# Kernel optimization log

Hardware: AMD Instinct MI355X
Metric: run time of the kernel (lower is better)

The kernel has to match this reference:

```python
import jax, jax.numpy as jnp
import numpy as np

B, S, D, H = 4, 8192, 1024, 16
HD = D // H  # head_dim = 64

def elu_feature_map(x):
    return jax.nn.elu(x) + 1.0

def setup_inputs() -> dict:
    key = jax.random.key(0)
    k1, k2, k3 = jax.random.split(key, 3)
    x = jax.random.normal(k1, (B, S, D), dtype=jnp.float32)
    w_qkv = jax.random.normal(k2, (3 * D, D), dtype=jnp.float32) * (D ** -0.5)
    w_out = jax.random.normal(k3, (D, D), dtype=jnp.float32) * (D ** -0.5)
    return {"x": x, "w_qkv": w_qkv, "w_out": w_out}

def reference(x, w_qkv, w_out):
    Bv, Sv, Dv = x.shape
    # qkv projection (torch Linear: x @ W.T), reshape to [3,B,H,S,hd]
    qkv = (x @ w_qkv.T).reshape(Bv, Sv, 3, H, HD)
    qkv = jnp.transpose(qkv, (2, 0, 3, 1, 4))
    q, k, v = qkv[0], qkv[1], qkv[2]
    q = elu_feature_map(q)
    k = elu_feature_map(k)
    # kv state: [B,H,hd,hd]
    kv = jnp.einsum('bhsd,bhse->bhde', k, v)
    out = jnp.einsum('bhsd,bhde->bhse', q, kv)
    k_sum = k.sum(axis=2)  # [B,H,hd]
    normalizer = jnp.einsum('bhsd,bhd->bhs', q, k_sum)[..., None]
    normalizer = jnp.maximum(normalizer, 1e-6)
    out = (out / normalizer).transpose(0, 2, 1, 3).reshape(Bv, Sv, Dv)
    return out @ w_out.T
```

## Files before the change

### kernel.cpp

```cpp
#include <hip/hip_runtime.h>
#include <cstdint>
#include <cstddef>


typedef __bf16 bf16;
typedef __bf16 bf16x8 __attribute__((ext_vector_type(8)));
typedef float  f32x4  __attribute__((ext_vector_type(4)));

#define MFMA(a, b, c) __builtin_amdgcn_mfma_f32_16x16x32_bf16((a), (b), (c), 0, 0, 0)

__device__ __forceinline__ void gld_lds16(const bf16* g, bf16* l) {
  __builtin_amdgcn_global_load_lds(
      (const __attribute__((address_space(1))) void*)g,
      (__attribute__((address_space(3))) void*)l, 16, 0, 0);
}

__global__ __launch_bounds__(256) void cvt_bf16(const float* __restrict__ src,
                                                bf16* __restrict__ dst, int n8) {
  const int stride = gridDim.x * 256;
  for (int i = blockIdx.x * 256 + threadIdx.x; i < n8; i += stride) {
    const float* p = src + (size_t)i * 8;
    f32x4 a = *(const f32x4*)p;
    f32x4 b = *(const f32x4*)(p + 4);
    bf16x8 r;
    r[0] = (bf16)a[0]; r[1] = (bf16)a[1]; r[2] = (bf16)a[2]; r[3] = (bf16)a[3];
    r[4] = (bf16)b[0]; r[5] = (bf16)b[1]; r[6] = (bf16)b[2]; r[7] = (bf16)b[3];
    *(bf16x8*)(dst + (size_t)i * 8) = r;
  }
}

template<int SLAB, bool ST, bool LAST>
__device__ __forceinline__ void ktile(
    const bf16* vA, const bf16* vB, bf16* sA, bf16* sB,
    const bf16* gA, const bf16* gB0, const bf16* gB1,
    f32x4 (&acc)[8][4]) {
  constexpr int NS = (SLAB + 2) % 3;
  constexpr int CB = SLAB * 12288;
  if (!LAST) asm volatile("s_waitcnt vmcnt(6)" ::: "memory");
  else       asm volatile("s_waitcnt vmcnt(0)" ::: "memory");
  __builtin_amdgcn_s_barrier();
  __builtin_amdgcn_sched_barrier(0);

  bf16x8 bv[4], af[4];
#pragma unroll
  for (int nf = 0; nf < 4; ++nf)
    bv[nf] = *(const bf16x8*)&vB[CB + nf * 512];
#pragma unroll
  for (int i = 0; i < 4; ++i)
    af[i] = *(const bf16x8*)&vA[CB + i * 512];
  if (ST) {
    gld_lds16(gA,         sA + NS * 12288);
    gld_lds16(gA + 65536, sA + NS * 12288 + 2048);
    gld_lds16(gB0,        sB + NS * 12288);
  }
  __builtin_amdgcn_s_barrier();
  asm volatile("s_waitcnt lgkmcnt(0)" ::: "memory");
  __builtin_amdgcn_sched_barrier(0);
  __builtin_amdgcn_s_setprio(1);
#pragma unroll
  for (int i = 0; i < 4; ++i)
#pragma unroll
    for (int nf = 0; nf < 4; ++nf)
      acc[i][nf] = MFMA(af[i], bv[nf], acc[i][nf]);
  __builtin_amdgcn_s_setprio(0);
  __builtin_amdgcn_s_barrier();

#pragma unroll
  for (int i = 0; i < 4; ++i)
    af[i] = *(const bf16x8*)&vA[CB + 2048 + i * 512];
  if (ST) {
    gld_lds16(gA + 131072, sA + NS * 12288 + 4096);
    gld_lds16(gA + 196608, sA + NS * 12288 + 6144);
    gld_lds16(gB1,         sB + NS * 12288 + 2048);
  }
  __builtin_amdgcn_s_barrier();
  asm volatile("s_waitcnt lgkmcnt(0)" ::: "memory");
  __builtin_amdgcn_sched_barrier(0);
  __builtin_amdgcn_s_setprio(1);
#pragma unroll
  for (int i = 0; i < 4; ++i)
#pragma unroll
    for (int nf = 0; nf < 4; ++nf)
      acc[4 + i][nf] = MFMA(af[i], bv[nf], acc[4 + i][nf]);
  __builtin_amdgcn_s_setprio(0);
  __builtin_amdgcn_s_barrier();
}

__device__ __forceinline__ void kloop(
    bf16* smem, const bf16* pA, const bf16* pB0, const bf16* pB1,
    int tid, int arow, int brow, int cgo, f32x4 (&acc)[8][4]) {
  bf16* sA = smem + tid * 8;
  bf16* sB = smem + 8192 + tid * 8;
#pragma unroll
  for (int t = 0; t < 2; ++t) {
    const int kk = t * 32;
    gld_lds16(pA + kk,          sA + t * 12288);
    gld_lds16(pA + kk + 65536,  sA + t * 12288 + 2048);
    gld_lds16(pA + kk + 131072, sA + t * 12288 + 4096);
    gld_lds16(pA + kk + 196608, sA + t * 12288 + 6144);
    gld_lds16(pB0 + kk,         sB + t * 12288);
    gld_lds16(pB1 + kk,         sB + t * 12288 + 2048);
  }
  const bf16* vA = smem + arow * 32 + cgo;
  const bf16* vB = smem + 8192 + brow * 32 + cgo;
#pragma unroll
  for (int c = 0; c < 10; ++c) {
    const int o = 64 + c * 96;
    ktile<0, true, false>(vA, vB, sA, sB, pA + o,      pB0 + o,      pB1 + o,      acc);
    ktile<1, true, false>(vA, vB, sA, sB, pA + o + 32, pB0 + o + 32, pB1 + o + 32, acc);
    ktile<2, true, false>(vA, vB, sA, sB, pA + o + 64, pB0 + o + 64, pB1 + o + 64, acc);
  }
  ktile<0, false, false>(vA, vB, sA, sB, pA, pB0, pB1, acc);
  ktile<1, false, true >(vA, vB, sA, sB, pA, pB0, pB1, acc);
}

__global__ __launch_bounds__(256, 2) void gemm_kvfold(
    const bf16* __restrict__ xb, const bf16* __restrict__ wbq,
    float* __restrict__ Pp, float* __restrict__ KsP) {
  __shared__ __align__(16) bf16 smem[36864];
  const int tid = threadIdx.x;
  const int w = tid >> 6, lane = tid & 63;
  const int grp = lane >> 4, mlane = lane & 15;
  const int wm = w >> 1, wn = w & 1;

  int bid = (int)blockIdx.x;
  const int cpx = (int)gridDim.x >> 3;
  bid = (bid & 7) * cpx + (bid >> 3);
  const int h = bid & 15, rt = bid >> 4;
  const int rowA0 = rt * 256;

  const int lrr = tid >> 2;
  const int lcs = (tid & 3) ^ ((tid >> 3) & 3);
  const bf16* pA  = xb + (size_t)(rowA0 + lrr) * 1024 + lcs * 8;
  const bf16* pB0 = wbq + (size_t)(1024 + h * 64 + lrr) * 1024 + lcs * 8;
  const bf16* pB1 = wbq + (size_t)(2048 + h * 64 + lrr) * 1024 + lcs * 8;
  const int cgo = (grp ^ ((mlane >> 1) & 3)) * 8;
  const int arow = wm * 128 + mlane;
  const int brow = wn * 64 + mlane;

  const f32x4 zero = {0.f, 0.f, 0.f, 0.f};
  f32x4 acc[8][4];
#pragma unroll
  for (int i = 0; i < 8; ++i)
#pragma unroll
    for (int j = 0; j < 4; ++j) acc[i][j] = zero;

  kloop(smem, pA, pB0, pB1, tid, arow, brow, cgo, acc);

  bf16* Kt = smem;
  bf16* Vt = smem + 17408;
  {
    bf16* T = wn ? Vt : Kt;
#pragma unroll
    for (int mf = 0; mf < 8; ++mf)
#pragma unroll
      for (int nf = 0; nf < 4; ++nf)
#pragma unroll
        for (int r = 0; r < 4; ++r) {
          float v = acc[mf][nf][r];
          if (wn == 0) v = (v > 0.f) ? (v + 1.f) : __expf(v);
          T[(wm * 128 + mf * 16 + grp * 4 + r) * 68 + nf * 16 + mlane] = (bf16)v;
        }
  }
  __syncthreads();

  f32x4 akv[4][4], a5[4];
#pragma unroll
  for (int i = 0; i < 4; ++i) {
    a5[i] = zero;
#pragma unroll
    for (int j = 0; j < 4; ++j) akv[i][j] = zero;
  }
  bf16x8 ones;
#pragma unroll
  for (int jj = 0; jj < 8; ++jj) ones[jj] = (bf16)1.0f;

#pragma unroll
  for (int c = 0; c < 2; ++c) {
    const int sw = w * 64 + c * 32;
    bf16x8 av[4], bk[4];
#pragma unroll
    for (int jj = 0; jj < 8; ++jj) {
      const bf16* vr = &Vt[(sw + grp * 8 + jj) * 68];
      const bf16* kr = &Kt[(sw + grp * 8 + jj) * 68];
#pragma unroll
      for (int i = 0; i < 4; ++i) av[i][jj] = vr[i * 16 + mlane];
#pragma unroll
      for (int j = 0; j < 4; ++j) bk[j][jj] = kr[j * 16 + mlane];
    }
#pragma unroll
    for (int i = 0; i < 4; ++i)
#pragma unroll
      for (int j = 0; j < 4; ++j) akv[i][j] = MFMA(av[i], bk[j], akv[i][j]);
#pragma unroll
    for (int j = 0; j < 4; ++j) a5[j] = MFMA(ones, bk[j], a5[j]);
  }
  __syncthreads();

  float* Pr = (float*)smem;
  float* Kr = Pr + 8192;
  if (w >= 2) {
#pragma unroll
    for (int i = 0; i < 4; ++i)
#pragma unroll
      for (int j = 0; j < 4; ++j)
#pragma unroll
        for (int r = 0; r < 4; ++r)
          Pr[(w - 2) * 4096 + (i * 16 + grp * 4 + r) * 64 + j * 16 + mlane] =
              akv[i][j][r];
    if (grp == 0) {
#pragma unroll
      for (int j = 0; j < 4; ++j) Kr[(w - 2) * 64 + j * 16 + mlane] = a5[j][0];
    }
  }
  __syncthreads();
  if (w < 2) {
#pragma unroll
    for (int i = 0; i < 4; ++i)
#pragma unroll
      for (int j = 0; j < 4; ++j)
#pragma unroll
        for (int r = 0; r < 4; ++r)
          akv[i][j][r] += Pr[w * 4096 + (i * 16 + grp * 4 + r) * 64 + j * 16 + mlane];
    if (grp == 0) {
#pragma unroll
      for (int j = 0; j < 4; ++j) a5[j][0] += Kr[w * 64 + j * 16 + mlane];
    }
  }
  __syncthreads();
  if (w == 1) {
#pragma unroll
    for (int i = 0; i < 4; ++i)
#pragma unroll
      for (int j = 0; j < 4; ++j)
#pragma unroll
        for (int r = 0; r < 4; ++r)
          Pr[(i * 16 + grp * 4 + r) * 64 + j * 16 + mlane] = akv[i][j][r];
    if (grp == 0) {
#pragma unroll
      for (int j = 0; j < 4; ++j) Kr[j * 16 + mlane] = a5[j][0];
    }
  }
  __syncthreads();
  if (w == 0) {
    const int widx = rt * 16 + h;
    float* pw = Pp + (size_t)widx * 4096;
#pragma unroll
    for (int i = 0; i < 4; ++i)
#pragma unroll
      for (int j = 0; j < 4; ++j)
#pragma unroll
        for (int r = 0; r < 4; ++r)
          pw[(i * 16 + grp * 4 + r) * 64 + j * 16 + mlane] =
              akv[i][j][r] + Pr[(i * 16 + grp * 4 + r) * 64 + j * 16 + mlane];
    if (grp == 0) {
#pragma unroll
      for (int j = 0; j < 4; ++j)
        KsP[(size_t)widx * 64 + j * 16 + mlane] =
            a5[j][0] + Kr[j * 16 + mlane];
    }
  }
}

__global__ __launch_bounds__(256) void reduce_kv2(
    const float* __restrict__ Pp, const float* __restrict__ KsP,
    bf16* __restrict__ kvb, bf16* __restrict__ ksb) {
  const int bh = blockIdx.x, y = blockIdx.y, tid = threadIdx.x;
  const int b = bh >> 4, h = bh & 15;
  if (y < 16) {
    const int o = y * 256 + tid;
    float s = 0.f;
#pragma unroll
    for (int i = 0; i < 32; ++i)
      s += Pp[(size_t)((b * 32 + i) * 16 + h) * 4096 + o];
    kvb[(size_t)bh * 4096 + o] = (bf16)s;
  } else if (tid < 64) {
    float s = 0.f;
#pragma unroll
    for (int i = 0; i < 32; ++i)
      s += KsP[(size_t)((b * 32 + i) * 16 + h) * 64 + tid];
    ksb[bh * 64 + tid] = (bf16)s;
  }
}

__global__ __launch_bounds__(256, 2) void gemm_qattn(
    const bf16* __restrict__ xb, const bf16* __restrict__ wbq,
    const bf16* __restrict__ kvb, const bf16* __restrict__ ksb,
    bf16* __restrict__ attn) {
  __shared__ __align__(16) bf16 smem[36864];
  const int tid = threadIdx.x;
  const int w = tid >> 6, lane = tid & 63;
  const int grp = lane >> 4, mlane = lane & 15;
  const int wm = w >> 1, wn = w & 1;

  int bid = (int)blockIdx.x;
  const int cpx = (int)gridDim.x >> 3;
  bid = (bid & 7) * cpx + (bid >> 3);
  const int ct = bid & 7, rt = bid >> 3;
  const int rowA0 = rt * 256;

  const int lrr = tid >> 2;
  const int lcs = (tid & 3) ^ ((tid >> 3) & 3);
  const bf16* pA  = xb + (size_t)(rowA0 + lrr) * 1024 + lcs * 8;
  const bf16* pB0 = wbq + (size_t)(ct * 128 + lrr) * 1024 + lcs * 8;
  const bf16* pB1 = pB0 + (size_t)64 * 1024;
  const int cgo = (grp ^ ((mlane >> 1) & 3)) * 8;
  const int arow = wm * 128 + mlane;
  const int brow = wn * 64 + mlane;

  const f32x4 zero = {0.f, 0.f, 0.f, 0.f};
  f32x4 acc[8][4];
#pragma unroll
  for (int i = 0; i < 8; ++i)
#pragma unroll
    for (int j = 0; j < 4; ++j) acc[i][j] = zero;

  kloop(smem, pA, pB0, pB1, tid, arow, brow, cgo, acc);

  const int head = ct * 2 + wn;
  const int bh = (rt >> 5) * 16 + head;
  bf16x8 bkv[2][4], b5v[2];
#pragma unroll
  for (int ks = 0; ks < 2; ++ks) {
#pragma unroll
    for (int nf = 0; nf < 4; ++nf)
      bkv[ks][nf] = *(const bf16x8*)&kvb[(size_t)bh * 4096 +
                                         (nf * 16 + mlane) * 64 + ks * 32 + grp * 8];
    b5v[ks] = *(const bf16x8*)&ksb[bh * 64 + ks * 32 + grp * 8];
  }

  bf16* Qs = smem + w * 4096;
  const int swr = (mlane >> 1) & 7;
#pragma unroll
  for (int mh = 0; mh < 2; ++mh) {
#pragma unroll
    for (int i = 0; i < 4; ++i)
#pragma unroll
      for (int nf = 0; nf < 4; ++nf)
#pragma unroll
        for (int r = 0; r < 4; ++r) {
          float v = acc[mh * 4 + i][nf][r];
          v = (v > 0.f) ? (v + 1.f) : __expf(v);
          const int rw = i * 16 + grp * 4 + r;
          const int d = nf * 16 + mlane;
          Qs[rw * 64 + (((d >> 3) ^ ((rw >> 1) & 7)) << 3) + (d & 7)] = (bf16)v;
        }
    bf16x8 aq2[4][2];
#pragma unroll
    for (int i = 0; i < 4; ++i)
#pragma unroll
      for (int ks = 0; ks < 2; ++ks)
        aq2[i][ks] = *(const bf16x8*)&Qs[(i * 16 + mlane) * 64 +
                                         (((ks * 4 + grp) ^ swr) << 3)];
    f32x4 ao[4][4], a5q[4];
#pragma unroll
    for (int i = 0; i < 4; ++i) {
      a5q[i] = zero;
#pragma unroll
      for (int nf = 0; nf < 4; ++nf) ao[i][nf] = zero;
    }
#pragma unroll
    for (int ks = 0; ks < 2; ++ks)
#pragma unroll
      for (int i = 0; i < 4; ++i) {
#pragma unroll
        for (int nf = 0; nf < 4; ++nf)
          ao[i][nf] = MFMA(aq2[i][ks], bkv[ks][nf], ao[i][nf]);
        a5q[i] = MFMA(aq2[i][ks], b5v[ks], a5q[i]);
      }
#pragma unroll
    for (int i = 0; i < 4; ++i)
#pragma unroll
      for (int r = 0; r < 4; ++r) {
        const float inv = 1.0f / fmaxf(a5q[i][r], 1e-6f);
        bf16* op = attn + (size_t)(rowA0 + wm * 128 + mh * 64 + i * 16 +
                                   grp * 4 + r) * 1024 + head * 64;
#pragma unroll
        for (int nf = 0; nf < 4; ++nf)
          op[nf * 16 + mlane] = (bf16)(ao[i][nf][r] * inv);
      }
  }
}

__global__ __launch_bounds__(256, 2) void gemm_out(
    const bf16* __restrict__ attn, const bf16* __restrict__ wbo,
    float* __restrict__ C) {
  __shared__ __align__(16) bf16 smem[36864];
  const int tid = threadIdx.x;
  const int w = tid >> 6, lane = tid & 63;
  const int grp = lane >> 4, mlane = lane & 15;
  const int wm = w >> 1, wn = w & 1;

  int bid = (int)blockIdx.x;
  const int cpx = (int)gridDim.x >> 3;
  bid = (bid & 7) * cpx + (bid >> 3);
  const int ct = bid & 7, rt = bid >> 3;
  const int rowA0 = rt * 256;

  const int lrr = tid >> 2;
  const int lcs = (tid & 3) ^ ((tid >> 3) & 3);
  const bf16* pA  = attn + (size_t)(rowA0 + lrr) * 1024 + lcs * 8;
  const bf16* pB0 = wbo + (size_t)(ct * 128 + lrr) * 1024 + lcs * 8;
  const bf16* pB1 = pB0 + (size_t)64 * 1024;
  const int cgo = (grp ^ ((mlane >> 1) & 3)) * 8;
  const int arow = wm * 128 + mlane;
  const int brow = wn * 64 + mlane;

  const f32x4 zero = {0.f, 0.f, 0.f, 0.f};
  f32x4 acc[8][4];
#pragma unroll
  for (int i = 0; i < 8; ++i)
#pragma unroll
    for (int j = 0; j < 4; ++j) acc[i][j] = zero;

  kloop(smem, pA, pB0, pB1, tid, arow, brow, cgo, acc);

#pragma unroll
  for (int mf = 0; mf < 8; ++mf)
#pragma unroll
    for (int nf = 0; nf < 4; ++nf) {
      float* cp = C + (size_t)(rowA0 + wm * 128 + mf * 16 + grp * 4) * 1024 +
                  ct * 128 + wn * 64 + nf * 16 + mlane;
#pragma unroll
      for (int r = 0; r < 4; ++r) cp[(size_t)r * 1024] = acc[mf][nf][r];
    }
}

extern "C" void kernel_launch(void* const* d_in, const int* in_sizes, int n_in,
                              void* d_out, int out_size, void* d_ws, size_t ws_size,
                              hipStream_t stream) {
  const float* x     = (const float*)d_in[0];
  const float* w_qkv = (const float*)d_in[1];
  const float* w_out = (const float*)d_in[2];
  char* O  = (char*)d_out;
  char* A  = (char*)d_in[0];
  char* W1 = (char*)d_in[1];

  bf16*  xb   = (bf16*)O;
  bf16*  wbq  = (bf16*)(O + 67108864);
  float* Pp   = (float*)(O + 75497472);
  float* KsP  = (float*)(O + 109051904);
  bf16*  attn = (bf16*)A;
  bf16*  wbo  = (bf16*)W1;
  bf16*  kvb  = (bf16*)(W1 + 2097152);
  bf16*  ksb  = (bf16*)(W1 + 2621440);

  cvt_bf16<<<2048, 256, 0, stream>>>(x, xb, 4194304);
  cvt_bf16<<<1536, 256, 0, stream>>>(w_qkv, wbq, 393216);
  cvt_bf16<<<512, 256, 0, stream>>>(w_out, wbo, 131072);
  gemm_kvfold<<<2048, 256, 0, stream>>>(xb, wbq, Pp, KsP);
  reduce_kv2<<<dim3(64, 17), 256, 0, stream>>>(Pp, KsP, kvb, ksb);
  gemm_qattn<<<1024, 256, 0, stream>>>(xb, wbq, kvb, ksb, attn);
  gemm_out<<<1024, 256, 0, stream>>>(attn, wbo, (float*)O);
}
```

Measured before the change: 535.3 us.

## Widen GEMM block tiles to 256x256 with 8 waves per block

All three GEMM kernels move from 256-thread blocks with 256x128 output tiles to 512-thread blocks with 256x256 tiles, using 8 waves in a 2x4 layout. The shared-memory staging is re-laid out to hold 256 B rows per slab, and each of the 512 threads issues 4 async loads per k-tile instead of 6. The kv-fold epilogue now loops over two heads per block and uses a deeper cross-wave reduction tree. The aim is to halve re-reads of the A operand and raise arithmetic intensity per block. The cost is larger LDS use (96 KB per block), which may limit occupancy, plus more barriers in the epilogue.

After: 571.5 us. +6.8%, slower.

```diff
diff --git a/kernel.cpp b/kernel.cpp
--- a/kernel.cpp
+++ b/kernel.cpp
@@ -30,13 +30,13 @@
 }
 
 template<int SLAB, bool ST, bool LAST>
-__device__ __forceinline__ void ktile(
-    const bf16* vA, const bf16* vB, bf16* sA, bf16* sB,
+__device__ __forceinline__ void ktile8(
+    const bf16* vA, const bf16* vB, bf16* sAd, bf16* sBd,
     const bf16* gA, const bf16* gB0, const bf16* gB1,
     f32x4 (&acc)[8][4]) {
   constexpr int NS = (SLAB + 2) % 3;
-  constexpr int CB = SLAB * 12288;
-  if (!LAST) asm volatile("s_waitcnt vmcnt(6)" ::: "memory");
+  constexpr int CB = SLAB * 16384;
+  if (!LAST) asm volatile("s_waitcnt vmcnt(4)" ::: "memory");
   else       asm volatile("s_waitcnt vmcnt(0)" ::: "memory");
   __builtin_amdgcn_s_barrier();
   __builtin_amdgcn_sched_barrier(0);
@@ -49,9 +49,8 @@
   for (int i = 0; i < 4; ++i)
     af[i] = *(const bf16x8*)&vA[CB + i * 512];
   if (ST) {
-    gld_lds16(gA,         sA + NS * 12288);
-    gld_lds16(gA + 65536, sA + NS * 12288 + 2048);
-    gld_lds16(gB0,        sB + NS * 12288);
+    gld_lds16(gA,          sAd + NS * 16384);
+    gld_lds16(gA + 131072, sAd + NS * 16384 + 4096);
   }
   __builtin_amdgcn_s_barrier();
   asm volatile("s_waitcnt lgkmcnt(0)" ::: "memory");
@@ -69,9 +68,8 @@
   for (int i = 0; i < 4; ++i)
     af[i] = *(const bf16x8*)&vA[CB + 2048 + i * 512];
   if (ST) {
-    gld_lds16(gA + 131072, sA + NS * 12288 + 4096);
-    gld_lds16(gA + 196608, sA + NS * 12288 + 6144);
-    gld_lds16(gB1,         sB + NS * 12288 + 2048);
+    gld_lds16(gB0, sBd + NS * 16384);
+    gld_lds16(gB1, sBd + NS * 16384 + 4096);
   }
   __builtin_amdgcn_s_barrier();
   asm volatile("s_waitcnt lgkmcnt(0)" ::: "memory");
@@ -86,57 +84,53 @@
   __builtin_amdgcn_s_barrier();
 }
 
-__device__ __forceinline__ void kloop(
+__device__ __forceinline__ void kloop8(
     bf16* smem, const bf16* pA, const bf16* pB0, const bf16* pB1,
-    int tid, int arow, int brow, int cgo, f32x4 (&acc)[8][4]) {
-  bf16* sA = smem + tid * 8;
-  bf16* sB = smem + 8192 + tid * 8;
+    int tid, const bf16* vA, const bf16* vB, f32x4 (&acc)[8][4]) {
+  bf16* sAd = smem + tid * 8;
+  bf16* sBd = smem + 8192 + tid * 8;
 #pragma unroll
   for (int t = 0; t < 2; ++t) {
     const int kk = t * 32;
-    gld_lds16(pA + kk,          sA + t * 12288);
-    gld_lds16(pA + kk + 65536,  sA + t * 12288 + 2048);
-    gld_lds16(pA + kk + 131072, sA + t * 12288 + 4096);
-    gld_lds16(pA + kk + 196608, sA + t * 12288 + 6144);
-    gld_lds16(pB0 + kk,         sB + t * 12288);
-    gld_lds16(pB1 + kk,         sB + t * 12288 + 2048);
-  }
-  const bf16* vA = smem + arow * 32 + cgo;
-  const bf16* vB = smem + 8192 + brow * 32 + cgo;
+    gld_lds16(pA + kk,          sAd + t * 16384);
+    gld_lds16(pA + kk + 131072, sAd + t * 16384 + 4096);
+    gld_lds16(pB0 + kk,         sBd + t * 16384);
+    gld_lds16(pB1 + kk,         sBd + t * 16384 + 4096);
+  }
 #pragma unroll
   for (int c = 0; c < 10; ++c) {
     const int o = 64 + c * 96;
-    ktile<0, true, false>(vA, vB, sA, sB, pA + o,      pB0 + o,      pB1 + o,      acc);
-    ktile<1, true, false>(vA, vB, sA, sB, pA + o + 32, pB0 + o + 32, pB1 + o + 32, acc);
-    ktile<2, true, false>(vA, vB, sA, sB, pA + o + 64, pB0 + o + 64, pB1 + o + 64, acc);
-  }
-  ktile<0, false, false>(vA, vB, sA, sB, pA, pB0, pB1, acc);
-  ktile<1, false, true >(vA, vB, sA, sB, pA, pB0, pB1, acc);
-}
-
-__global__ __launch_bounds__(256, 2) void gemm_kvfold(
+    ktile8<0, true, false>(vA, vB, sAd, sBd, pA + o,      pB0 + o,      pB1 + o,      acc);
+    ktile8<1, true, false>(vA, vB, sAd, sBd, pA + o + 32, pB0 + o + 32, pB1 + o + 32, acc);
+    ktile8<2, true, false>(vA, vB, sAd, sBd, pA + o + 64, pB0 + o + 64, pB1 + o + 64, acc);
+  }
+  ktile8<0, false, false>(vA, vB, sAd, sBd, pA, pB0, pB1, acc);
+  ktile8<1, false, true >(vA, vB, sAd, sBd, pA, pB0, pB1, acc);
+}
+
+__global__ __launch_bounds__(512, 2) void gemm_kvfold(
     const bf16* __restrict__ xb, const bf16* __restrict__ wbq,
     float* __restrict__ Pp, float* __restrict__ KsP) {
-  __shared__ __align__(16) bf16 smem[36864];
+  __shared__ __align__(16) bf16 smem[49152];
   const int tid = threadIdx.x;
   const int w = tid >> 6, lane = tid & 63;
   const int grp = lane >> 4, mlane = lane & 15;
-  const int wm = w >> 1, wn = w & 1;
+  const int wm = w >> 2, wn = w & 3;
 
   int bid = (int)blockIdx.x;
   const int cpx = (int)gridDim.x >> 3;
   bid = (bid & 7) * cpx + (bid >> 3);
-  const int h = bid & 15, rt = bid >> 4;
+  const int hp = bid & 7, rt = bid >> 3;
   const int rowA0 = rt * 256;
 
   const int lrr = tid >> 2;
   const int lcs = (tid & 3) ^ ((tid >> 3) & 3);
   const bf16* pA  = xb + (size_t)(rowA0 + lrr) * 1024 + lcs * 8;
-  const bf16* pB0 = wbq + (size_t)(1024 + h * 64 + lrr) * 1024 + lcs * 8;
-  const bf16* pB1 = wbq + (size_t)(2048 + h * 64 + lrr) * 1024 + lcs * 8;
+  const bf16* pB0 = wbq + (size_t)(1024 + hp * 128 + lrr) * 1024 + lcs * 8;
+  const bf16* pB1 = wbq + (size_t)(2048 + hp * 128 + lrr) * 1024 + lcs * 8;
   const int cgo = (grp ^ ((mlane >> 1) & 3)) * 8;
-  const int arow = wm * 128 + mlane;
-  const int brow = wn * 64 + mlane;
+  const bf16* vA = smem + (wm * 128 + mlane) * 32 + cgo;
+  const bf16* vB = smem + 8192 + (wn * 64 + mlane) * 32 + cgo;
 
   const f32x4 zero = {0.f, 0.f, 0.f, 0.f};
   f32x4 acc[8][4];
@@ -145,119 +139,153 @@
 #pragma unroll
     for (int j = 0; j < 4; ++j) acc[i][j] = zero;
 
-  kloop(smem, pA, pB0, pB1, tid, arow, brow, cgo, acc);
+  kloop8(smem, pA, pB0, pB1, tid, vA, vB, acc);
 
   bf16* Kt = smem;
   bf16* Vt = smem + 17408;
-  {
-    bf16* T = wn ? Vt : Kt;
-#pragma unroll
-    for (int mf = 0; mf < 8; ++mf)
-#pragma unroll
-      for (int nf = 0; nf < 4; ++nf)
-#pragma unroll
-        for (int r = 0; r < 4; ++r) {
-          float v = acc[mf][nf][r];
-          if (wn == 0) v = (v > 0.f) ? (v + 1.f) : __expf(v);
-          T[(wm * 128 + mf * 16 + grp * 4 + r) * 68 + nf * 16 + mlane] = (bf16)v;
-        }
-  }
-  __syncthreads();
-
-  f32x4 akv[4][4], a5[4];
-#pragma unroll
-  for (int i = 0; i < 4; ++i) {
-    a5[i] = zero;
-#pragma unroll
-    for (int j = 0; j < 4; ++j) akv[i][j] = zero;
-  }
+  float* P4 = (float*)smem;
+  float* K4 = (float*)((char*)smem + 65536);
   bf16x8 ones;
 #pragma unroll
   for (int jj = 0; jj < 8; ++jj) ones[jj] = (bf16)1.0f;
 
 #pragma unroll
-  for (int c = 0; c < 2; ++c) {
-    const int sw = w * 64 + c * 32;
-    bf16x8 av[4], bk[4];
-#pragma unroll
-    for (int jj = 0; jj < 8; ++jj) {
-      const bf16* vr = &Vt[(sw + grp * 8 + jj) * 68];
-      const bf16* kr = &Kt[(sw + grp * 8 + jj) * 68];
-#pragma unroll
-      for (int i = 0; i < 4; ++i) av[i][jj] = vr[i * 16 + mlane];
-#pragma unroll
-      for (int j = 0; j < 4; ++j) bk[j][jj] = kr[j * 16 + mlane];
-    }
-#pragma unroll
-    for (int i = 0; i < 4; ++i)
-#pragma unroll
-      for (int j = 0; j < 4; ++j) akv[i][j] = MFMA(av[i], bk[j], akv[i][j]);
-#pragma unroll
-    for (int j = 0; j < 4; ++j) a5[j] = MFMA(ones, bk[j], a5[j]);
-  }
-  __syncthreads();
-
-  float* Pr = (float*)smem;
-  float* Kr = Pr + 8192;
-  if (w >= 2) {
-#pragma unroll
-    for (int i = 0; i < 4; ++i)
-#pragma unroll
-      for (int j = 0; j < 4; ++j)
-#pragma unroll
-        for (int r = 0; r < 4; ++r)
-          Pr[(w - 2) * 4096 + (i * 16 + grp * 4 + r) * 64 + j * 16 + mlane] =
-              akv[i][j][r];
-    if (grp == 0) {
-#pragma unroll
-      for (int j = 0; j < 4; ++j) Kr[(w - 2) * 64 + j * 16 + mlane] = a5[j][0];
-    }
-  }
-  __syncthreads();
-  if (w < 2) {
-#pragma unroll
-    for (int i = 0; i < 4; ++i)
-#pragma unroll
-      for (int j = 0; j < 4; ++j)
-#pragma unroll
-        for (int r = 0; r < 4; ++r)
-          akv[i][j][r] += Pr[w * 4096 + (i * 16 + grp * 4 + r) * 64 + j * 16 + mlane];
-    if (grp == 0) {
-#pragma unroll
-      for (int j = 0; j < 4; ++j) a5[j][0] += Kr[w * 64 + j * 16 + mlane];
-    }
-  }
-  __syncthreads();
-  if (w == 1) {
-#pragma unroll
-    for (int i = 0; i < 4; ++i)
-#pragma unroll
-      for (int j = 0; j < 4; ++j)
-#pragma unroll
-        for (int r = 0; r < 4; ++r)
-          Pr[(i * 16 + grp * 4 + r) * 64 + j * 16 + mlane] = akv[i][j][r];
-    if (grp == 0) {
-#pragma unroll
-      for (int j = 0; j < 4; ++j) Kr[j * 16 + mlane] = a5[j][0];
-    }
-  }
-  __syncthreads();
-  if (w == 0) {
-    const int widx = rt * 16 + h;
-    float* pw = Pp + (size_t)widx * 4096;
-#pragma unroll
-    for (int i = 0; i < 4; ++i)
-#pragma unroll
-      for (int j = 0; j < 4; ++j)
-#pragma unroll
-        for (int r = 0; r < 4; ++r)
-          pw[(i * 16 + grp * 4 + r) * 64 + j * 16 + mlane] =
-              akv[i][j][r] + Pr[(i * 16 + grp * 4 + r) * 64 + j * 16 + mlane];
-    if (grp == 0) {
-#pragma unroll
-      for (int j = 0; j < 4; ++j)
-        KsP[(size_t)widx * 64 + j * 16 + mlane] =
-            a5[j][0] + Kr[j * 16 + mlane];
+  for (int h = 0; h < 2; ++h) {
+    __syncthreads();
+    if (wn == h || wn == 2 + h) {
+      const bool isk = (wn == h);
+      bf16* T = isk ? Kt : Vt;
+#pragma unroll
+      for (int mf = 0; mf < 8; ++mf)
+#pragma unroll
+        for (int nf = 0; nf < 4; ++nf)
+#pragma unroll
+          for (int r = 0; r < 4; ++r) {
+            float v = acc[mf][nf][r];
+            if (isk) v = (v > 0.f) ? (v + 1.f) : __expf(v);
+            T[(wm * 128 + mf * 16 + grp * 4 + r) * 68 + nf * 16 + mlane] = (bf16)v;
+          }
+    }
+    __syncthreads();
+
+    f32x4 akv[4][4], a5[4];
+#pragma unroll
+    for (int i = 0; i < 4; ++i) {
+      a5[i] = zero;
+#pragma unroll
+      for (int j = 0; j < 4; ++j) akv[i][j] = zero;
+    }
+    {
+      const int sw = w * 32;
+      bf16x8 av[4], bk[4];
+#pragma unroll
+      for (int jj = 0; jj < 8; ++jj) {
+        const bf16* vr = &Vt[(sw + grp * 8 + jj) * 68];
+        const bf16* kr = &Kt[(sw + grp * 8 + jj) * 68];
+#pragma unroll
+        for (int i = 0; i < 4; ++i) av[i][jj] = vr[i * 16 + mlane];
+#pragma unroll
+        for (int j = 0; j < 4; ++j) bk[j][jj] = kr[j * 16 + mlane];
+      }
+#pragma unroll
+      for (int i = 0; i < 4; ++i)
+#pragma unroll
+        for (int j = 0; j < 4; ++j) akv[i][j] = MFMA(av[i], bk[j], akv[i][j]);
+#pragma unroll
+      for (int j = 0; j < 4; ++j) a5[j] = MFMA(ones, bk[j], a5[j]);
+    }
+    __syncthreads();
+
+    if (w >= 4) {
+#pragma unroll
+      for (int i = 0; i < 4; ++i)
+#pragma unroll
+        for (int j = 0; j < 4; ++j)
+#pragma unroll
+          for (int r = 0; r < 4; ++r)
+            P4[(w - 4) * 4096 + (i * 16 + grp * 4 + r) * 64 + j * 16 + mlane] =
+                akv[i][j][r];
+      if (grp == 0) {
+#pragma unroll
+        for (int j = 0; j < 4; ++j) K4[(w - 4) * 64 + j * 16 + mlane] = a5[j][0];
+      }
+    }
+    __syncthreads();
+    if (w < 4) {
+#pragma unroll
+      for (int i = 0; i < 4; ++i)
+#pragma unroll
+        for (int j = 0; j < 4; ++j)
+#pragma unroll
+          for (int r = 0; r < 4; ++r)
+            akv[i][j][r] += P4[w * 4096 + (i * 16 + grp * 4 + r) * 64 + j * 16 + mlane];
+      if (grp == 0) {
+#pragma unroll
+        for (int j = 0; j < 4; ++j) a5[j][0] += K4[w * 64 + j * 16 + mlane];
+      }
+    }
+    __syncthreads();
+    if (w == 2 || w == 3) {
+#pragma unroll
+      for (int i = 0; i < 4; ++i)
+#pragma unroll
+        for (int j = 0; j < 4; ++j)
+#pragma unroll
+          for (int r = 0; r < 4; ++r)
+            P4[(w - 2) * 4096 + (i * 16 + grp * 4 + r) * 64 + j * 16 + mlane] =
+                akv[i][j][r];
+      if (grp == 0) {
+#pragma unroll
+        for (int j = 0; j < 4; ++j) K4[(w - 2) * 64 + j * 16 + mlane] = a5[j][0];
+      }
+    }
+    __syncthreads();
+    if (w < 2) {
+#pragma unroll
+      for (int i = 0; i < 4; ++i)
+#pragma unroll
+        for (int j = 0; j < 4; ++j)
+#pragma unroll
+          for (int r = 0; r < 4; ++r)
+            akv[i][j][r] += P4[w * 4096 + (i * 16 + grp * 4 + r) * 64 + j * 16 + mlane];
+      if (grp == 0) {
+#pragma unroll
+        for (int j = 0; j < 4; ++j) a5[j][0] += K4[w * 64 + j * 16 + mlane];
+      }
+    }
+    __syncthreads();
+    if (w == 1) {
+#pragma unroll
+      for (int i = 0; i < 4; ++i)
+#pragma unroll
+        for (int j = 0; j < 4; ++j)
+#pragma unroll
+          for (int r = 0; r < 4; ++r)
+            P4[4096 + (i * 16 + grp * 4 + r) * 64 + j * 16 + mlane] = akv[i][j][r];
+      if (grp == 0) {
+#pragma unroll
+        for (int j = 0; j < 4; ++j) K4[64 + j * 16 + mlane] = a5[j][0];
+      }
+    }
+    __syncthreads();
+    if (w == 0) {
+      const int widx = rt * 16 + hp * 2 + h;
+      float* pw = Pp + (size_t)widx * 4096;
+#pragma unroll
+      for (int i = 0; i < 4; ++i)
+#pragma unroll
+        for (int j = 0; j < 4; ++j)
+#pragma unroll
+          for (int r = 0; r < 4; ++r)
+            pw[(i * 16 + grp * 4 + r) * 64 + j * 16 + mlane] =
+                akv[i][j][r] +
+                P4[4096 + (i * 16 + grp * 4 + r) * 64 + j * 16 + mlane];
+      if (grp == 0) {
+#pragma unroll
+        for (int j = 0; j < 4; ++j)
+          KsP[(size_t)widx * 64 + j * 16 + mlane] =
+              a5[j][0] + K4[64 + j * 16 + mlane];
+      }
     }
   }
 }
@@ -283,30 +311,30 @@
   }
 }
 
-__global__ __launch_bounds__(256, 2) void gemm_qattn(
+__global__ __launch_bounds__(512, 2) void gemm_qattn(
     const bf16* __restrict__ xb, const bf16* __restrict__ wbq,
     const bf16* __restrict__ kvb, const bf16* __restrict__ ksb,
     bf16* __restrict__ attn) {
-  __shared__ __align__(16) bf16 smem[36864];
+  __shared__ __align__(16) bf16 smem[49152];
   const int tid = threadIdx.x;
   const int w = tid >> 6, lane = tid & 63;
   const int grp = lane >> 4, mlane = lane & 15;
-  const int wm = w >> 1, wn = w & 1;
+  const int wm = w >> 2, wn = w & 3;
 
   int bid = (int)blockIdx.x;
   const int cpx = (int)gridDim.x >> 3;
   bid = (bid & 7) * cpx + (bid >> 3);
-  const int ct = bid & 7, rt = bid >> 3;
+  const int ct = bid & 3, rt = bid >> 2;
   const int rowA0 = rt * 256;
 
   const int lrr = tid >> 2;
   const int lcs = (tid & 3) ^ ((tid >> 3) & 3);
   const bf16* pA  = xb + (size_t)(rowA0 + lrr) * 1024 + lcs * 8;
-  const bf16* pB0 = wbq + (size_t)(ct * 128 + lrr) * 1024 + lcs * 8;
-  const bf16* pB1 = pB0 + (size_t)64 * 1024;
+  const bf16* pB0 = wbq + (size_t)(ct * 256 + lrr) * 1024 + lcs * 8;
+  const bf16* pB1 = pB0 + (size_t)128 * 1024;
   const int cgo = (grp ^ ((mlane >> 1) & 3)) * 8;
-  const int arow = wm * 128 + mlane;
-  const int brow = wn * 64 + mlane;
+  const bf16* vA = smem + (wm * 128 + mlane) * 32 + cgo;
+  const bf16* vB = smem + 8192 + (wn * 64 + mlane) * 32 + cgo;
 
   const f32x4 zero = {0.f, 0.f, 0.f, 0.f};
   f32x4 acc[8][4];
@@ -315,9 +343,9 @@
 #pragma unroll
     for (int j = 0; j < 4; ++j) acc[i][j] = zero;
 
-  kloop(smem, pA, pB0, pB1, tid, arow, brow, cgo, acc);
-
-  const int head = ct * 2 + wn;
+  kloop8(smem, pA, pB0, pB1, tid, vA, vB, acc);
+
+  const int head = ct * 4 + wn;
   const int bh = (rt >> 5) * 16 + head;
   bf16x8 bkv[2][4], b5v[2];
 #pragma unroll
@@ -382,29 +410,29 @@
   }
 }
 
-__global__ __launch_bounds__(256, 2) void gemm_out(
+__global__ __launch_bounds__(512, 2) void gemm_out(
     const bf16* __restrict__ attn, const bf16* __restrict__ wbo,
     float* __restrict__ C) {
-  __shared__ __align__(16) bf16 smem[36864];
+  __shared__ __align__(16) bf16 smem[49152];
   const int tid = threadIdx.x;
   const int w = tid >> 6, lane = tid & 63;
   const int grp = lane >> 4, mlane = lane & 15;
-  const int wm = w >> 1, wn = w & 1;
+  const int wm = w >> 2, wn = w & 3;
 
   int bid = (int)blockIdx.x;
   const int cpx = (int)gridDim.x >> 3;
   bid = (bid & 7) * cpx + (bid >> 3);
-  const int ct = bid & 7, rt = bid >> 3;
+  const int ct = bid & 3, rt = bid >> 2;
   const int rowA0 = rt * 256;
 
   const int lrr = tid >> 2;
   const int lcs = (tid & 3) ^ ((tid >> 3) & 3);
   const bf16* pA  = attn + (size_t)(rowA0 + lrr) * 1024 + lcs * 8;
-  const bf16* pB0 = wbo + (size_t)(ct * 128 + lrr) * 1024 + lcs * 8;
-  const bf16* pB1 = pB0 + (size_t)64 * 1024;
+  const bf16* pB0 = wbo + (size_t)(ct * 256 + lrr) * 1024 + lcs * 8;
+  const bf16* pB1 = pB0 + (size_t)128 * 1024;
   const int cgo = (grp ^ ((mlane >> 1) & 3)) * 8;
-  const int arow = wm * 128 + mlane;
-  const int brow = wn * 64 + mlane;
+  const bf16* vA = smem + (wm * 128 + mlane) * 32 + cgo;
+  const bf16* vB = smem + 8192 + (wn * 64 + mlane) * 32 + cgo;
 
   const f32x4 zero = {0.f, 0.f, 0.f, 0.f};
   f32x4 acc[8][4];
@@ -413,14 +441,14 @@
 #pragma unroll
     for (int j = 0; j < 4; ++j) acc[i][j] = zero;
 
-  kloop(smem, pA, pB0, pB1, tid, arow, brow, cgo, acc);
+  kloop8(smem, pA, pB0, pB1, tid, vA, vB, acc);
 
 #pragma unroll
   for (int mf = 0; mf < 8; ++mf)
 #pragma unroll
     for (int nf = 0; nf < 4; ++nf) {
       float* cp = C + (size_t)(rowA0 + wm * 128 + mf * 16 + grp * 4) * 1024 +
-                  ct * 128 + wn * 64 + nf * 16 + mlane;
+                  ct * 256 + wn * 64 + nf * 16 + mlane;
 #pragma unroll
       for (int r = 0; r < 4; ++r) cp[(size_t)r * 1024] = acc[mf][nf][r];
     }
@@ -448,8 +476,8 @@
   cvt_bf16<<<2048, 256, 0, stream>>>(x, xb, 4194304);
   cvt_bf16<<<1536, 256, 0, stream>>>(w_qkv, wbq, 393216);
   cvt_bf16<<<512, 256, 0, stream>>>(w_out, wbo, 131072);
-  gemm_kvfold<<<2048, 256, 0, stream>>>(xb, wbq, Pp, KsP);
+  gemm_kvfold<<<1024, 512, 0, stream>>>(xb, wbq, Pp, KsP);
   reduce_kv2<<<dim3(64, 17), 256, 0, stream>>>(Pp, KsP, kvb, ksb);
-  gemm_qattn<<<1024, 256, 0, stream>>>(xb, wbq, kvb, ksb, attn);
-  gemm_out<<<1024, 256, 0, stream>>>(attn, wbo, (float*)O);
-}
+  gemm_qattn<<<512, 512, 0, stream>>>(xb, wbq, kvb, ksb, attn);
+  gemm_out<<<512, 512, 0, stream>>>(attn, wbo, (float*)O);
+}
```
